# Kernel optimization log

Hardware: AMD Instinct MI355X
Metric: run time of the kernel (lower is better)

Reference implementation:

```python
import jax, jax.numpy as jnp
import numpy as np

D_MODEL = 1024


def setup_inputs() -> dict:
    key = jax.random.key(0)
    kx, kq, kk, kv = jax.random.split(key, 4)
    x = jax.random.normal(kx, (4, 2048, D_MODEL), dtype=jnp.float32)
    s = 1.0 / np.sqrt(D_MODEL)
    # torch nn.Linear weight is [out, in]; y = x @ W.T
    Wq = jax.random.normal(kq, (D_MODEL, D_MODEL), dtype=jnp.float32) * s
    Wk = jax.random.normal(kk, (D_MODEL, D_MODEL), dtype=jnp.float32) * s
    Wv = jax.random.normal(kv, (D_MODEL, D_MODEL), dtype=jnp.float32) * s
    return {"x": x, "Wq": Wq, "Wk": Wk, "Wv": Wv}


def reference(x, Wq, Wk, Wv):
    # Linear projections (no bias): [b, s, d]
    Q = jnp.einsum("bsd,ed->bse", x, Wq)
    K = jnp.einsum("bsd,ed->bse", x, Wk)
    V = jnp.einsum("bsd,ed->bse", x, Wv)
    d_k = Q.shape[-1]
    scores = jnp.einsum("bqd,bkd->bqk", Q, K) / jnp.sqrt(jnp.asarray(d_k, Q.dtype))
    weights = jax.nn.softmax(scores, axis=-1)
    return jnp.einsum("bqk,bkd->bqd", weights, V)
```

## Files before the change

kernel.cpp:

```cpp
#include <hip/hip_runtime.h>
#include <hip/hip_bf16.h>

using bf16 = __hip_bfloat16;
typedef __attribute__((ext_vector_type(8))) short short8;
typedef __attribute__((ext_vector_type(16))) float f32x16;

__global__ __launch_bounds__(256) void cast_all(const float* __restrict__ x,
                                                const float* __restrict__ Wq,
                                                const float* __restrict__ Wk,
                                                const float* __restrict__ Wv,
                                                bf16* __restrict__ xb, bf16* __restrict__ Wb) {
  const int b = blockIdx.x;
  const float* src;
  bf16* dst;
  if (b < 8192) {
    src = x + (size_t)b * 1024;
    dst = xb + (size_t)b * 1024;
  } else if (b < 9216) {
    src = Wq + (size_t)(b - 8192) * 1024;
    dst = Wb + (size_t)(b - 8192) * 1024;
  } else if (b < 10240) {
    src = Wk + (size_t)(b - 9216) * 1024;
    dst = Wb + (size_t)(b - 8192) * 1024;
  } else {
    src = Wv + (size_t)(b - 10240) * 1024;
    dst = Wb + (size_t)(b - 8192) * 1024;
  }
  const int i = threadIdx.x * 4;
  const float4 f = *(const float4*)(src + i);
  bf16 h[4];
  h[0] = __float2bfloat16(f.x);
  h[1] = __float2bfloat16(f.y);
  h[2] = __float2bfloat16(f.z);
  h[3] = __float2bfloat16(f.w);
  *(uint2*)(dst + i) = *(const uint2*)h;
}

template <int BK, int SMEM_BYTES, class Epi>
__device__ __forceinline__ void gemm_nt(const bf16* __restrict__ A, const bf16* __restrict__ B,
                                        int lda, int ldb, int K, int m0, int n0, Epi epi) {
  constexpr int KS = BK / 16;
  constexpr int CPR = BK / 8;
  constexpr int SH = (BK == 32) ? 2 : 3;
  constexpr int N_INSTR = 128 * CPR / 256;
  __shared__ char smem[SMEM_BYTES];
  bf16* As = (bf16*)smem;
  bf16* Bs = (bf16*)(smem + 128 * BK * 2);
  const int t = threadIdx.x;
  const int lane = t & 63;
  const int wave = t >> 6;
  const int wm = (wave >> 1) * 64;
  const int wn = (wave & 1) * 64;

  f32x16 acc[2][2];
#pragma unroll
  for (int i = 0; i < 2; ++i)
#pragma unroll
    for (int j = 0; j < 2; ++j)
#pragma unroll
      for (int r = 0; r < 16; ++r) acc[i][j][r] = 0.f;

  const bf16* gA[N_INSTR];
  const bf16* gB[N_INSTR];
#pragma unroll
  for (int j = 0; j < N_INSTR; ++j) {
    const int slot = j * 256 + t;
    const int row = slot >> SH;
    const int f = (row + (row >> SH)) & (CPR - 1);
    const int c = ((slot & (CPR - 1)) ^ f) << 3;
    gA[j] = A + (size_t)(m0 + row) * lda + c;
    gB[j] = B + (size_t)(n0 + row) * ldb + c;
  }

  const int rl = lane & 31;
  const int grp = lane >> 5;

  for (int k0 = 0; k0 < K; k0 += BK) {
#pragma unroll
    for (int j = 0; j < N_INSTR; ++j) {
      __builtin_amdgcn_global_load_lds(
          (const __attribute__((address_space(1))) unsigned int*)(gA[j] + k0),
          (__attribute__((address_space(3))) unsigned int*)(As + (j * 256 + wave * 64) * 8), 16, 0, 0);
      __builtin_amdgcn_global_load_lds(
          (const __attribute__((address_space(1))) unsigned int*)(gB[j] + k0),
          (__attribute__((address_space(3))) unsigned int*)(Bs + (j * 256 + wave * 64) * 8), 16, 0, 0);
    }
    __syncthreads();

    short8 af[KS][2], bv[KS][2];
#pragma unroll
    for (int ks = 0; ks < KS; ++ks) {
      const int kb = ks * 2 + grp;
#pragma unroll
      for (int mt = 0; mt < 2; ++mt) {
        const int rowa = wm + mt * 32 + rl;
        const int fa = (rowa + (rowa >> SH)) & (CPR - 1);
        af[ks][mt] = *(const short8*)(As + rowa * BK + ((kb ^ fa) << 3));
        const int rowb = wn + mt * 32 + rl;
        const int fb = (rowb + (rowb >> SH)) & (CPR - 1);
        bv[ks][mt] = *(const short8*)(Bs + rowb * BK + ((kb ^ fb) << 3));
      }
    }
#pragma unroll
    for (int ks = 0; ks < KS; ++ks)
#pragma unroll
      for (int mt = 0; mt < 2; ++mt)
#pragma unroll
        for (int nt = 0; nt < 2; ++nt)
          acc[mt][nt] = __builtin_amdgcn_mfma_f32_32x32x16_bf16(af[ks][mt], bv[ks][nt],
                                                                acc[mt][nt], 0, 0, 0);
    __syncthreads();
  }

  epi(acc, m0, n0, wm, wn, lane, wave, smem);
}

__device__ __forceinline__ int c_row(int reg, int lane) {
  return (reg & 3) + 8 * (reg >> 2) + 4 * (lane >> 5);
}

template <class F>
__device__ __forceinline__ void for_each_c(const f32x16 (&acc)[2][2], int wm, int wn, int lane,
                                           F f) {
  const int rl = lane & 31;
#pragma unroll
  for (int mt = 0; mt < 2; ++mt)
#pragma unroll
    for (int nt = 0; nt < 2; ++nt)
#pragma unroll
      for (int reg = 0; reg < 16; ++reg)
        f(wm + mt * 32 + c_row(reg, lane), wn + nt * 32 + rl, acc[mt][nt][reg]);
}

__global__ __launch_bounds__(256) void proj_kernel(const bf16* __restrict__ xb,
                                                   const bf16* __restrict__ Wb,
                                                   bf16* __restrict__ Qb, bf16* __restrict__ Kb,
                                                   bf16* __restrict__ Vt) {
  const int id = blockIdx.y * 24 + blockIdx.x;
  const int g = id & 7, s = id >> 3;
  const int m0 = (g * 8 + (s & 7)) * 128;
  const int n0 = (s >> 3) * 128;
  gemm_nt<32, 18432>(xb, Wb, 1024, 1024, 1024, m0, n0,
             [=](const f32x16 (&acc)[2][2], int m0, int n0, int wm, int wn, int lane, int wave,
                 char* smem) {
    if (n0 < 2048) {
      bf16* dst = (n0 < 1024) ? Qb : Kb;
      const int nb = (n0 < 1024) ? n0 : (n0 - 1024);
      for_each_c(acc, wm, wn, lane, [&](int m, int n, float v) {
        dst[(size_t)(m0 + m) * 1024 + nb + n] = __float2bfloat16(v);
      });
    } else {
      bf16* T = (bf16*)(smem) + wave * 2304;
      const int rl = lane & 31;
      const int g4 = 4 * (lane >> 5);
      const int mbase = m0 + wm;
      const int bb = mbase >> 11;
      const int sbase = mbase & 2047;
      const int nvbase = n0 - 2048 + wn;
#pragma unroll
      for (int p = 0; p < 2; ++p) {
#pragma unroll
        for (int mt = 0; mt < 2; ++mt)
#pragma unroll
          for (int q = 0; q < 4; ++q) {
            bf16 h4[4];
#pragma unroll
            for (int r = 0; r < 4; ++r) h4[r] = __float2bfloat16(acc[mt][p][4 * q + r]);
            *(uint2*)(T + rl * 72 + mt * 32 + 8 * q + g4) = *(const uint2*)h4;
          }
        asm volatile("s_waitcnt lgkmcnt(0)" ::: "memory");
#pragma unroll
        for (int i = 0; i < 4; ++i) {
          const int nl = i * 8 + (lane >> 3);
          const int ml = (lane & 7) * 8;
          const short8 val = *(const short8*)(T + nl * 72 + ml);
          *(short8*)(Vt + ((size_t)bb * 1024 + nvbase + p * 32 + nl) * 2048 + sbase + ml) = val;
        }
        asm volatile("s_waitcnt lgkmcnt(0)" ::: "memory");
      }
    }
  });
}

__global__ __launch_bounds__(256) void qk_exp_kernel(const bf16* __restrict__ Qb,
                                                     const bf16* __restrict__ Kb,
                                                     bf16* __restrict__ E,
                                                     float* __restrict__ Lpart) {
  const int z = blockIdx.z;
  const int id2 = blockIdx.y * 16 + blockIdx.x;
  const int g = id2 & 7, s = id2 >> 3;
  const int m0 = ((g & 3) * 4 + (s & 3)) * 128;
  const int n0 = ((g >> 2) * 8 + (s >> 2)) * 128;
  const bf16* A = Qb + (size_t)z * 2048 * 1024;
  const bf16* B = Kb + (size_t)z * 2048 * 1024;
  bf16* Ez = E + (size_t)z * 2048 * 2048;
  float* Lz = Lpart + (size_t)z * 16 * 2048;
  gemm_nt<64, 32768>(A, B, 1024, 1024, 1024, m0, n0,
             [=](const f32x16 (&acc)[2][2], int m0, int n0, int wm, int wn, int lane, int wave,
                 char* smem) {
    float* Lp = (float*)smem;
    const int rl = lane & 31;
#pragma unroll
    for (int mt = 0; mt < 2; ++mt)
#pragma unroll
      for (int reg = 0; reg < 16; ++reg) {
        const int mr = wm + mt * 32 + c_row(reg, lane);
        float s2 = 0.f;
#pragma unroll
        for (int nt = 0; nt < 2; ++nt) {
          const float e = __expf(acc[mt][nt][reg] * 0.03125f);
          Ez[(size_t)(m0 + mr) * 2048 + n0 + wn + nt * 32 + rl] = __float2bfloat16(e);
          s2 += e;
        }
        s2 += __shfl_xor(s2, 1, 64);
        s2 += __shfl_xor(s2, 2, 64);
        s2 += __shfl_xor(s2, 4, 64);
        s2 += __shfl_xor(s2, 8, 64);
        s2 += __shfl_xor(s2, 16, 64);
        if (rl == 0) Lp[mr * 2 + (wave & 1)] = s2;
      }
    __syncthreads();
    const int t = threadIdx.x;
    if (t < 128) Lz[(n0 >> 7) * 2048 + m0 + t] = Lp[t * 2 + 0] + Lp[t * 2 + 1];
  });
}

__global__ __launch_bounds__(256) void pv_kernel(const bf16* __restrict__ E,
                                                 const bf16* __restrict__ Vt,
                                                 const float* __restrict__ Lpart,
                                                 float* __restrict__ out) {
  const int z = blockIdx.z;
  const int id2 = blockIdx.y * 8 + blockIdx.x;
  const int g = id2 & 7, s = id2 >> 3;
  const int m0 = ((g & 3) * 4 + (s & 3)) * 128;
  const int n0 = ((g >> 2) * 4 + (s >> 2)) * 128;
  const bf16* A = E + (size_t)z * 2048 * 2048;
  const bf16* B = Vt + (size_t)z * 1024 * 2048;
  const float* Lz = Lpart + (size_t)z * 16 * 2048;
  float* oz = out + (size_t)z * 2048 * 1024;
  gemm_nt<64, 32768>(A, B, 2048, 2048, 2048, m0, n0,
             [=](const f32x16 (&acc)[2][2], int m0, int n0, int wm, int wn, int lane, int wave,
                 char* smem) {
    float* Lsm = (float*)smem;
    const int t = threadIdx.x;
    if (t < 128) {
      float s2 = 0.f;
#pragma unroll
      for (int i = 0; i < 16; ++i) s2 += Lz[(size_t)i * 2048 + m0 + t];
      Lsm[t] = 1.f / s2;
    }
    __syncthreads();
    const int rl = lane & 31;
#pragma unroll
    for (int mt = 0; mt < 2; ++mt)
#pragma unroll
      for (int reg = 0; reg < 16; ++reg) {
        const int ml = wm + mt * 32 + c_row(reg, lane);
        const float il = Lsm[ml];
#pragma unroll
        for (int nt = 0; nt < 2; ++nt)
          oz[(size_t)(m0 + ml) * 1024 + n0 + wn + nt * 32 + rl] = acc[mt][nt][reg] * il;
      }
  });
}

extern "C" void kernel_launch(void* const* d_in, const int* in_sizes, int n_in,
                              void* d_out, int out_size, void* d_ws, size_t ws_size,
                              hipStream_t stream) {
  const float* x = (const float*)d_in[0];
  const float* Wq = (const float*)d_in[1];
  const float* Wk = (const float*)d_in[2];
  const float* Wv = (const float*)d_in[3];
  float* out = (float*)d_out;

  char* w = (char*)d_ws;
  bf16* xb = (bf16*)w; w += (size_t)8192 * 1024 * 2;
  bf16* Wb = (bf16*)w; w += (size_t)3072 * 1024 * 2;
  bf16* Qb = (bf16*)w; w += (size_t)8192 * 1024 * 2;
  bf16* Kb = (bf16*)w; w += (size_t)8192 * 1024 * 2;
  bf16* Vt = (bf16*)w; w += (size_t)8192 * 1024 * 2;
  bf16* E  = (bf16*)w; w += (size_t)4 * 2048 * 2048 * 2;
  float* Lpart = (float*)w; w += (size_t)4 * 16 * 2048 * 4;

  cast_all<<<11264, 256, 0, stream>>>(x, Wq, Wk, Wv, xb, Wb);

  proj_kernel<<<dim3(24, 64), 256, 0, stream>>>(xb, Wb, Qb, Kb, Vt);

  qk_exp_kernel<<<dim3(16, 16, 4), 256, 0, stream>>>(Qb, Kb, E, Lpart);

  pv_kernel<<<dim3(8, 16, 4), 256, 0, stream>>>(E, Vt, Lpart, out);
}
```

Measured before the change: 251.2 us.

## Replace 128x128 GEMM core with 256x256 eight-wave multi-stage pipelined GEMM

Replaces the single-buffered 128x128 tile GEMM with a 256x256 tile, 512-thread kernel that keeps a 4-slot LDS ring buffer. Loads run three k-steps ahead, and compute is split into half-k phases with barriers, setprio and sched_barrier so global-to-LDS loads overlap MFMA work. Larger tiles cut redundant global traffic, and the prefetch is meant to hide load latency that the old load-sync-compute loop exposed. All three GEMM kernels and their epilogues, grids and the partial softmax-sum layout are adapted to match. The cost is fewer blocks, which hurts wave quantization on the smaller grids, plus heavy LDS use (128KB) and more register pressure.

```diff
diff --git a/kernel.cpp b/kernel.cpp
--- a/kernel.cpp
+++ b/kernel.cpp
@@ -36,83 +36,97 @@
   *(uint2*)(dst + i) = *(const uint2*)h;
 }
 
-template <int BK, int SMEM_BYTES, class Epi>
-__device__ __forceinline__ void gemm_nt(const bf16* __restrict__ A, const bf16* __restrict__ B,
+#define GPHASE(AS, BS, Q, S0, S1, VM)                                          \
+  do {                                                                         \
+    short8 af[4], bv[2];                                                       \
+    _Pragma("unroll") for (int mt = 0; mt < 4; ++mt) {                         \
+      const int row = wr * 128 + mt * 32 + rl;                                 \
+      const int fz = (row + (row >> 2)) & 3;                                   \
+      af[mt] = *(const short8*)((AS) + row * 32 + ((((Q)*2 + grp) ^ fz) << 3));\
+    }                                                                          \
+    _Pragma("unroll") for (int nt = 0; nt < 2; ++nt) {                         \
+      const int row = wc * 64 + nt * 32 + rl;                                  \
+      const int fz = (row + (row >> 2)) & 3;                                   \
+      bv[nt] = *(const short8*)((BS) + row * 32 + ((((Q)*2 + grp) ^ fz) << 3));\
+    }                                                                          \
+    S0;                                                                        \
+    S1;                                                                        \
+    VM;                                                                        \
+    __builtin_amdgcn_s_barrier();                                              \
+    asm volatile("s_waitcnt lgkmcnt(0)" ::: "memory");                         \
+    __builtin_amdgcn_sched_barrier(0);                                         \
+    __builtin_amdgcn_s_setprio(1);                                             \
+    _Pragma("unroll") for (int mt = 0; mt < 4; ++mt)                           \
+      _Pragma("unroll") for (int nt = 0; nt < 2; ++nt)                         \
+        acc[mt][nt] = __builtin_amdgcn_mfma_f32_32x32x16_bf16(af[mt], bv[nt],  \
+                                                              acc[mt][nt], 0, 0, 0); \
+    __builtin_amdgcn_s_setprio(0);                                             \
+    __builtin_amdgcn_s_barrier();                                              \
+  } while (0)
+
+template <class Epi>
+__device__ __forceinline__ void gemm256(const bf16* __restrict__ A, const bf16* __restrict__ B,
                                         int lda, int ldb, int K, int m0, int n0, Epi epi) {
-  constexpr int KS = BK / 16;
-  constexpr int CPR = BK / 8;
-  constexpr int SH = (BK == 32) ? 2 : 3;
-  constexpr int N_INSTR = 128 * CPR / 256;
-  __shared__ char smem[SMEM_BYTES];
-  bf16* As = (bf16*)smem;
-  bf16* Bs = (bf16*)(smem + 128 * BK * 2);
+  __shared__ char smem[131072];
   const int t = threadIdx.x;
   const int lane = t & 63;
   const int wave = t >> 6;
-  const int wm = (wave >> 1) * 64;
-  const int wn = (wave & 1) * 64;
-
-  f32x16 acc[2][2];
-#pragma unroll
-  for (int i = 0; i < 2; ++i)
-#pragma unroll
-    for (int j = 0; j < 2; ++j)
-#pragma unroll
-      for (int r = 0; r < 16; ++r) acc[i][j][r] = 0.f;
-
-  const bf16* gA[N_INSTR];
-  const bf16* gB[N_INSTR];
-#pragma unroll
-  for (int j = 0; j < N_INSTR; ++j) {
-    const int slot = j * 256 + t;
-    const int row = slot >> SH;
-    const int f = (row + (row >> SH)) & (CPR - 1);
-    const int c = ((slot & (CPR - 1)) ^ f) << 3;
-    gA[j] = A + (size_t)(m0 + row) * lda + c;
-    gB[j] = B + (size_t)(n0 + row) * ldb + c;
-  }
-
+  const int wr = wave >> 2;
+  const int wc = wave & 3;
   const int rl = lane & 31;
   const int grp = lane >> 5;
 
-  for (int k0 = 0; k0 < K; k0 += BK) {
-#pragma unroll
-    for (int j = 0; j < N_INSTR; ++j) {
-      __builtin_amdgcn_global_load_lds(
-          (const __attribute__((address_space(1))) unsigned int*)(gA[j] + k0),
-          (__attribute__((address_space(3))) unsigned int*)(As + (j * 256 + wave * 64) * 8), 16, 0, 0);
-      __builtin_amdgcn_global_load_lds(
-          (const __attribute__((address_space(1))) unsigned int*)(gB[j] + k0),
-          (__attribute__((address_space(3))) unsigned int*)(Bs + (j * 256 + wave * 64) * 8), 16, 0, 0);
-    }
-    __syncthreads();
-
-    short8 af[KS][2], bv[KS][2];
-#pragma unroll
-    for (int ks = 0; ks < KS; ++ks) {
-      const int kb = ks * 2 + grp;
-#pragma unroll
-      for (int mt = 0; mt < 2; ++mt) {
-        const int rowa = wm + mt * 32 + rl;
-        const int fa = (rowa + (rowa >> SH)) & (CPR - 1);
-        af[ks][mt] = *(const short8*)(As + rowa * BK + ((kb ^ fa) << 3));
-        const int rowb = wn + mt * 32 + rl;
-        const int fb = (rowb + (rowb >> SH)) & (CPR - 1);
-        bv[ks][mt] = *(const short8*)(Bs + rowb * BK + ((kb ^ fb) << 3));
-      }
-    }
-#pragma unroll
-    for (int ks = 0; ks < KS; ++ks)
-#pragma unroll
-      for (int mt = 0; mt < 2; ++mt)
-#pragma unroll
-        for (int nt = 0; nt < 2; ++nt)
-          acc[mt][nt] = __builtin_amdgcn_mfma_f32_32x32x16_bf16(af[ks][mt], bv[ks][nt],
-                                                                acc[mt][nt], 0, 0, 0);
-    __syncthreads();
+  f32x16 acc[4][2];
+#pragma unroll
+  for (int i = 0; i < 4; ++i)
+#pragma unroll
+    for (int j = 0; j < 2; ++j)
+#pragma unroll
+      for (int r = 0; r < 16; ++r) acc[i][j][r] = 0.f;
+
+  const bf16* gA[2];
+  const bf16* gB[2];
+#pragma unroll
+  for (int h = 0; h < 2; ++h) {
+    const int row = h * 128 + (t >> 2);
+    const int fz = (row + (row >> 2)) & 3;
+    const int c = ((t & 3) ^ fz) << 3;
+    gA[h] = A + (size_t)(m0 + row) * lda + c;
+    gB[h] = B + (size_t)(n0 + row) * ldb + c;
   }
 
-  epi(acc, m0, n0, wm, wn, lane, wave, smem);
+  const int NT = K >> 5;
+
+  auto stageA = [&](int kt, int h) {
+    char* dst = smem + (((kt & 3) * 2048 + h * 512 + wave * 64) << 4);
+    __builtin_amdgcn_global_load_lds(
+        (const __attribute__((address_space(1))) unsigned int*)(gA[h] + kt * 32),
+        (__attribute__((address_space(3))) unsigned int*)dst, 16, 0, 0);
+  };
+  auto stageB = [&](int kt, int h) {
+    char* dst = smem + (((kt & 3) * 2048 + 1024 + h * 512 + wave * 64) << 4);
+    __builtin_amdgcn_global_load_lds(
+        (const __attribute__((address_space(1))) unsigned int*)(gB[h] + kt * 32),
+        (__attribute__((address_space(3))) unsigned int*)dst, 16, 0, 0);
+  };
+
+  stageA(0, 0); stageB(0, 0); stageA(0, 1); stageB(0, 1);
+  stageA(1, 0); stageB(1, 0); stageA(1, 1); stageB(1, 1);
+  stageA(2, 0); stageB(2, 0); stageA(2, 1); stageB(2, 1);
+  asm volatile("s_waitcnt vmcnt(8)" ::: "memory");
+  __builtin_amdgcn_s_barrier();
+
+  for (int kt = 0; kt < NT; ++kt) {
+    const bf16* As = (const bf16*)(smem + (kt & 3) * 32768);
+    const bf16* Bs = (const bf16*)(smem + (kt & 3) * 32768 + 16384);
+    const bool pre = (kt + 3 < NT);
+    GPHASE(As, Bs, 0, if (pre) stageA(kt + 3, 0), if (pre) stageB(kt + 3, 0), ((void)0));
+    GPHASE(As, Bs, 1, if (pre) stageA(kt + 3, 1), if (pre) stageB(kt + 3, 1),
+           asm volatile("s_waitcnt vmcnt(8)" ::: "memory"));
+  }
+  __syncthreads();
+
+  epi(acc, m0, n0, wr, wc, lane, (char*)smem);
 }
 
 __device__ __forceinline__ int c_row(int reg, int lane) {
@@ -120,60 +134,61 @@
 }
 
 template <class F>
-__device__ __forceinline__ void for_each_c(const f32x16 (&acc)[2][2], int wm, int wn, int lane,
+__device__ __forceinline__ void for_each_c(const f32x16 (&acc)[4][2], int wr, int wc, int lane,
                                            F f) {
   const int rl = lane & 31;
 #pragma unroll
-  for (int mt = 0; mt < 2; ++mt)
+  for (int mt = 0; mt < 4; ++mt)
 #pragma unroll
     for (int nt = 0; nt < 2; ++nt)
 #pragma unroll
       for (int reg = 0; reg < 16; ++reg)
-        f(wm + mt * 32 + c_row(reg, lane), wn + nt * 32 + rl, acc[mt][nt][reg]);
-}
-
-__global__ __launch_bounds__(256) void proj_kernel(const bf16* __restrict__ xb,
-                                                   const bf16* __restrict__ Wb,
-                                                   bf16* __restrict__ Qb, bf16* __restrict__ Kb,
-                                                   bf16* __restrict__ Vt) {
-  const int id = blockIdx.y * 24 + blockIdx.x;
+        f(wr * 128 + mt * 32 + c_row(reg, lane), wc * 64 + nt * 32 + rl, acc[mt][nt][reg]);
+}
+
+__global__ __launch_bounds__(512, 2) void proj_kernel(const bf16* __restrict__ xb,
+                                                      const bf16* __restrict__ Wb,
+                                                      bf16* __restrict__ Qb,
+                                                      bf16* __restrict__ Kb,
+                                                      bf16* __restrict__ Vt) {
+  const int id = blockIdx.x;
   const int g = id & 7, s = id >> 3;
-  const int m0 = (g * 8 + (s & 7)) * 128;
-  const int n0 = (s >> 3) * 128;
-  gemm_nt<32, 18432>(xb, Wb, 1024, 1024, 1024, m0, n0,
-             [=](const f32x16 (&acc)[2][2], int m0, int n0, int wm, int wn, int lane, int wave,
-                 char* smem) {
+  const int m0 = (g * 4 + (s & 3)) * 256;
+  const int n0 = (s >> 2) * 256;
+  gemm256(xb, Wb, 1024, 1024, 1024, m0, n0,
+          [=](const f32x16 (&acc)[4][2], int m0, int n0, int wr, int wc, int lane, char* smem) {
     if (n0 < 2048) {
       bf16* dst = (n0 < 1024) ? Qb : Kb;
-      const int nb = (n0 < 1024) ? n0 : (n0 - 1024);
-      for_each_c(acc, wm, wn, lane, [&](int m, int n, float v) {
+      const int nb = n0 & 1023;
+      for_each_c(acc, wr, wc, lane, [&](int m, int n, float v) {
         dst[(size_t)(m0 + m) * 1024 + nb + n] = __float2bfloat16(v);
       });
     } else {
-      bf16* T = (bf16*)(smem) + wave * 2304;
+      const int wave = threadIdx.x >> 6;
+      bf16* T = (bf16*)smem + wave * 4352;
       const int rl = lane & 31;
       const int g4 = 4 * (lane >> 5);
-      const int mbase = m0 + wm;
+      const int mbase = m0 + wr * 128;
       const int bb = mbase >> 11;
       const int sbase = mbase & 2047;
-      const int nvbase = n0 - 2048 + wn;
+      const int nvbase = n0 - 2048 + wc * 64;
 #pragma unroll
       for (int p = 0; p < 2; ++p) {
 #pragma unroll
-        for (int mt = 0; mt < 2; ++mt)
+        for (int mt = 0; mt < 4; ++mt)
 #pragma unroll
           for (int q = 0; q < 4; ++q) {
             bf16 h4[4];
 #pragma unroll
             for (int r = 0; r < 4; ++r) h4[r] = __float2bfloat16(acc[mt][p][4 * q + r]);
-            *(uint2*)(T + rl * 72 + mt * 32 + 8 * q + g4) = *(const uint2*)h4;
+            *(uint2*)(T + rl * 136 + mt * 32 + 8 * q + g4) = *(const uint2*)h4;
           }
         asm volatile("s_waitcnt lgkmcnt(0)" ::: "memory");
 #pragma unroll
-        for (int i = 0; i < 4; ++i) {
-          const int nl = i * 8 + (lane >> 3);
-          const int ml = (lane & 7) * 8;
-          const short8 val = *(const short8*)(T + nl * 72 + ml);
+        for (int i = 0; i < 8; ++i) {
+          const int nl = i * 4 + (lane >> 4);
+          const int ml = (lane & 15) * 8;
+          const short8 val = *(const short8*)(T + nl * 136 + ml);
           *(short8*)(Vt + ((size_t)bb * 1024 + nvbase + p * 32 + nl) * 2048 + sbase + ml) = val;
         }
         asm volatile("s_waitcnt lgkmcnt(0)" ::: "memory");
@@ -182,34 +197,33 @@
   });
 }
 
-__global__ __launch_bounds__(256) void qk_exp_kernel(const bf16* __restrict__ Qb,
-                                                     const bf16* __restrict__ Kb,
-                                                     bf16* __restrict__ E,
-                                                     float* __restrict__ Lpart) {
-  const int z = blockIdx.z;
-  const int id2 = blockIdx.y * 16 + blockIdx.x;
+__global__ __launch_bounds__(512, 2) void qk_exp_kernel(const bf16* __restrict__ Qb,
+                                                        const bf16* __restrict__ Kb,
+                                                        bf16* __restrict__ E,
+                                                        float* __restrict__ Lpart) {
+  const int z = blockIdx.y;
+  const int id2 = blockIdx.x;
   const int g = id2 & 7, s = id2 >> 3;
-  const int m0 = ((g & 3) * 4 + (s & 3)) * 128;
-  const int n0 = ((g >> 2) * 8 + (s >> 2)) * 128;
+  const int m0 = ((g & 3) * 2 + (s & 1)) * 256;
+  const int n0 = ((g >> 2) * 4 + (s >> 1)) * 256;
   const bf16* A = Qb + (size_t)z * 2048 * 1024;
   const bf16* B = Kb + (size_t)z * 2048 * 1024;
   bf16* Ez = E + (size_t)z * 2048 * 2048;
-  float* Lz = Lpart + (size_t)z * 16 * 2048;
-  gemm_nt<64, 32768>(A, B, 1024, 1024, 1024, m0, n0,
-             [=](const f32x16 (&acc)[2][2], int m0, int n0, int wm, int wn, int lane, int wave,
-                 char* smem) {
+  float* Lz = Lpart + (size_t)z * 8 * 2048;
+  gemm256(A, B, 1024, 1024, 1024, m0, n0,
+          [=](const f32x16 (&acc)[4][2], int m0, int n0, int wr, int wc, int lane, char* smem) {
     float* Lp = (float*)smem;
     const int rl = lane & 31;
 #pragma unroll
-    for (int mt = 0; mt < 2; ++mt)
+    for (int mt = 0; mt < 4; ++mt)
 #pragma unroll
       for (int reg = 0; reg < 16; ++reg) {
-        const int mr = wm + mt * 32 + c_row(reg, lane);
+        const int mr = wr * 128 + mt * 32 + c_row(reg, lane);
         float s2 = 0.f;
 #pragma unroll
         for (int nt = 0; nt < 2; ++nt) {
           const float e = __expf(acc[mt][nt][reg] * 0.03125f);
-          Ez[(size_t)(m0 + mr) * 2048 + n0 + wn + nt * 32 + rl] = __float2bfloat16(e);
+          Ez[(size_t)(m0 + mr) * 2048 + n0 + wc * 64 + nt * 32 + rl] = __float2bfloat16(e);
           s2 += e;
         }
         s2 += __shfl_xor(s2, 1, 64);
@@ -217,49 +231,49 @@
         s2 += __shfl_xor(s2, 4, 64);
         s2 += __shfl_xor(s2, 8, 64);
         s2 += __shfl_xor(s2, 16, 64);
-        if (rl == 0) Lp[mr * 2 + (wave & 1)] = s2;
+        if (rl == 0) Lp[mr * 4 + wc] = s2;
       }
     __syncthreads();
     const int t = threadIdx.x;
-    if (t < 128) Lz[(n0 >> 7) * 2048 + m0 + t] = Lp[t * 2 + 0] + Lp[t * 2 + 1];
+    if (t < 256)
+      Lz[(n0 >> 8) * 2048 + m0 + t] = Lp[t * 4 + 0] + Lp[t * 4 + 1] + Lp[t * 4 + 2] + Lp[t * 4 + 3];
   });
 }
 
-__global__ __launch_bounds__(256) void pv_kernel(const bf16* __restrict__ E,
-                                                 const bf16* __restrict__ Vt,
-                                                 const float* __restrict__ Lpart,
-                                                 float* __restrict__ out) {
-  const int z = blockIdx.z;
-  const int id2 = blockIdx.y * 8 + blockIdx.x;
+__global__ __launch_bounds__(512, 2) void pv_kernel(const bf16* __restrict__ E,
+                                                    const bf16* __restrict__ Vt,
+                                                    const float* __restrict__ Lpart,
+                                                    float* __restrict__ out) {
+  const int z = blockIdx.y;
+  const int id2 = blockIdx.x;
   const int g = id2 & 7, s = id2 >> 3;
-  const int m0 = ((g & 3) * 4 + (s & 3)) * 128;
-  const int n0 = ((g >> 2) * 4 + (s >> 2)) * 128;
+  const int m0 = ((g & 3) * 2 + (s & 1)) * 256;
+  const int n0 = ((g >> 2) * 2 + (s >> 1)) * 256;
   const bf16* A = E + (size_t)z * 2048 * 2048;
   const bf16* B = Vt + (size_t)z * 1024 * 2048;
-  const float* Lz = Lpart + (size_t)z * 16 * 2048;
+  const float* Lz = Lpart + (size_t)z * 8 * 2048;
   float* oz = out + (size_t)z * 2048 * 1024;
-  gemm_nt<64, 32768>(A, B, 2048, 2048, 2048, m0, n0,
-             [=](const f32x16 (&acc)[2][2], int m0, int n0, int wm, int wn, int lane, int wave,
-                 char* smem) {
+  gemm256(A, B, 2048, 2048, 2048, m0, n0,
+          [=](const f32x16 (&acc)[4][2], int m0, int n0, int wr, int wc, int lane, char* smem) {
     float* Lsm = (float*)smem;
     const int t = threadIdx.x;
-    if (t < 128) {
+    if (t < 256) {
       float s2 = 0.f;
 #pragma unroll
-      for (int i = 0; i < 16; ++i) s2 += Lz[(size_t)i * 2048 + m0 + t];
+      for (int i = 0; i < 8; ++i) s2 += Lz[(size_t)i * 2048 + m0 + t];
       Lsm[t] = 1.f / s2;
     }
     __syncthreads();
     const int rl = lane & 31;
 #pragma unroll
-    for (int mt = 0; mt < 2; ++mt)
+    for (int mt = 0; mt < 4; ++mt)
 #pragma unroll
       for (int reg = 0; reg < 16; ++reg) {
-        const int ml = wm + mt * 32 + c_row(reg, lane);
+        const int ml = wr * 128 + mt * 32 + c_row(reg, lane);
         const float il = Lsm[ml];
 #pragma unroll
         for (int nt = 0; nt < 2; ++nt)
-          oz[(size_t)(m0 + ml) * 1024 + n0 + wn + nt * 32 + rl] = acc[mt][nt][reg] * il;
+          oz[(size_t)(m0 + ml) * 1024 + n0 + wc * 64 + nt * 32 + rl] = acc[mt][nt][reg] * il;
       }
   });
 }
@@ -280,13 +294,13 @@
   bf16* Kb = (bf16*)w; w += (size_t)8192 * 1024 * 2;
   bf16* Vt = (bf16*)w; w += (size_t)8192 * 1024 * 2;
   bf16* E  = (bf16*)w; w += (size_t)4 * 2048 * 2048 * 2;
-  float* Lpart = (float*)w; w += (size_t)4 * 16 * 2048 * 4;
+  float* Lpart = (float*)w; w += (size_t)4 * 8 * 2048 * 4;
 
   cast_all<<<11264, 256, 0, stream>>>(x, Wq, Wk, Wv, xb, Wb);
 
-  proj_kernel<<<dim3(24, 64), 256, 0, stream>>>(xb, Wb, Qb, Kb, Vt);
-
-  qk_exp_kernel<<<dim3(16, 16, 4), 256, 0, stream>>>(Qb, Kb, E, Lpart);
-
-  pv_kernel<<<dim3(8, 16, 4), 256, 0, stream>>>(E, Vt, Lpart, out);
-}
+  proj_kernel<<<384, 512, 0, stream>>>(xb, Wb, Qb, Kb, Vt);
+
+  qk_exp_kernel<<<dim3(64, 4), 512, 0, stream>>>(Qb, Kb, E, Lpart);
+
+  pv_kernel<<<dim3(32, 4), 512, 0, stream>>>(E, Vt, Lpart, out);
+}
```

New measurement: 261.6 us. +4.1%, slower.
